# Performance work log

Hardware: AMD Instinct MI355X
Metric: run time of the kernel (lower is better)

## Reference

```python
import jax, jax.numpy as jnp
import numpy as np

VOCAB, HIDDEN, BATCH, TLEN = 32000, 512, 32, 64


def _lstm_cell(x, h, c, Wih, Whh, bih, bhh):
    # PyTorch LSTMCell gate order: i, f, g, o
    g = x @ Wih.T + bih + h @ Whh.T + bhh  # [B, 4H]
    i, f, gg, o = jnp.split(g, 4, axis=-1)
    i = jax.nn.sigmoid(i)
    f = jax.nn.sigmoid(f)
    gg = jnp.tanh(gg)
    o = jax.nn.sigmoid(o)
    c2 = f * c + i * gg
    h2 = o * jnp.tanh(c2)
    return h2, c2


def setup_inputs() -> dict:
    key = jax.random.key(0)
    ks = jax.random.split(key, 16)
    s = 0.02
    inp = {
        "inputs": jax.random.randint(ks[0], (1, BATCH), 0, VOCAB),
        "hiddens": jax.random.normal(ks[1], (BATCH, HIDDEN), jnp.float32),
        "target_sequences": jax.random.randint(ks[2], (BATCH, TLEN), 0, VOCAB),
        "use_tf": 1,
        "emb": jax.random.normal(ks[3], (VOCAB, HIDDEN), jnp.float32) * s,
        "W_ih1": jax.random.normal(ks[4], (4 * HIDDEN, HIDDEN), jnp.float32) * s,
        "W_hh1": jax.random.normal(ks[5], (4 * HIDDEN, HIDDEN), jnp.float32) * s,
        "b_ih1": jax.random.normal(ks[6], (4 * HIDDEN,), jnp.float32) * s,
        "b_hh1": jax.random.normal(ks[7], (4 * HIDDEN,), jnp.float32) * s,
        "W_ih2": jax.random.normal(ks[8], (4 * HIDDEN, HIDDEN), jnp.float32) * s,
        "W_hh2": jax.random.normal(ks[9], (4 * HIDDEN, HIDDEN), jnp.float32) * s,
        "b_ih2": jax.random.normal(ks[10], (4 * HIDDEN,), jnp.float32) * s,
        "b_hh2": jax.random.normal(ks[11], (4 * HIDDEN,), jnp.float32) * s,
        "W_out": jax.random.normal(ks[12], (VOCAB, HIDDEN), jnp.float32) * s,
        "b_out": jax.random.normal(ks[13], (VOCAB,), jnp.float32) * s,
    }
    return inp


def reference(inputs, hiddens, target_sequences, use_tf, emb, W_ih1, W_hh1,
              b_ih1, b_hh1, W_ih2, W_hh2, b_ih2, b_hh2, W_out, b_out):
    # Teacher-forcing path (use_tf is a static Python int; dropout p=0 -> identity).
    B = inputs.shape[1]
    H = hiddens.shape[1]
    # step i consumes: emb(inputs) for i=0, emb(target[:, i-1]) for i>0
    e0 = emb[inputs[0]]                              # [B, H]
    et = emb[target_sequences.T[:-1]]                # [T-1, B, H]
    x_seq = jnp.concatenate([e0[None], et], axis=0)  # [T, B, H]

    c1 = jnp.zeros((B, H), hiddens.dtype)
    h2 = jnp.zeros((B, H), hiddens.dtype)
    c2 = jnp.zeros((B, H), hiddens.dtype)

    def step(carry, x):
        h1, c1, h2, c2 = carry
        h1, c1 = _lstm_cell(x, h1, c1, W_ih1, W_hh1, b_ih1, b_hh1)
        h2, c2 = _lstm_cell(h1, h2, c2, W_ih2, W_hh2, b_ih2, b_hh2)
        probs = jax.nn.softmax(h2 @ W_out.T + b_out, axis=-1)  # [B, V]
        return (h1, c1, h2, c2), probs

    (h1, c1, h2, c2), output = jax.lax.scan(step, (hiddens, c1, h2, c2), x_seq)
    return output, h1  # output: [T, B, V]
```

## Files before the change

kernel.cpp:

```cpp
#include <hip/hip_runtime.h>
#include <stdint.h>


constexpr int kH = 512;
constexpr int kB = 32;
constexpr int kT = 64;
constexpr int kV = 32000;
constexpr int kG = 2048;
constexpr int kNWG = 256;
constexpr int kWS = 129;

typedef __attribute__((ext_vector_type(4))) float f4;
typedef __attribute__((ext_vector_type(8))) short short8;
typedef unsigned long long u64;

struct us4 { unsigned short x, y, z, w; };

__device__ inline unsigned short f2bf(float x) {
  union { float f; unsigned u; } c; c.f = x;
  unsigned r = c.u + 0x7fffu + ((c.u >> 16) & 1u);
  return (unsigned short)(r >> 16);
}
__device__ inline float sigm(float x) { return 1.0f / (1.0f + expf(-x)); }

__global__ void k_init(float* __restrict__ buf2, float* __restrict__ rowsum,
                       int* __restrict__ flags ) {
  int id = blockIdx.x * 256 + threadIdx.x;
  f4 z = {0.f, 0.f, 0.f, 0.f};
  if (id < 8192) ((f4*)buf2)[id] = z;
  if (id < 2048) rowsum[id] = 0.f;
  if (id < 512)  flags[id] = 0;
}

__global__ void k_wcvt(const float* __restrict__ W, unsigned short* __restrict__ Wu) {
  const int total = kV * kH / 4;
  for (int i = blockIdx.x * blockDim.x + threadIdx.x; i < total;
       i += gridDim.x * blockDim.x) {
    f4 v = ((const f4*)W)[i];
    us4 o = {f2bf(v.x), f2bf(v.y), f2bf(v.z), f2bf(v.w)};
    ((us4*)Wu)[i] = o;
  }
}

__global__ __launch_bounds__(256) void k_xg1(
    const int* __restrict__ inputs, const int* __restrict__ tseq,
    const float* __restrict__ emb, const float* __restrict__ Wih1,
    const float* __restrict__ bih1, const float* __restrict__ bhh1,
    float* __restrict__ Xg1T) {
  __shared__ float Xs[kB * kH];
  int tid = threadIdx.x;
  int t = blockIdx.x, jb = blockIdx.y;
  for (int i = tid; i < kB * kH / 4; i += 256) {
    int b = i >> 7;
    int tok = (t == 0) ? inputs[b] : tseq[b * kT + (t - 1)];
    ((f4*)Xs)[i] = ((const f4*)(emb + (size_t)tok * kH))[i & 127];
  }
  __syncthreads();
  int j2 = tid & 31, bq = tid >> 5;
  int j0 = jb * 64 + j2 * 2;
  int b0 = bq * 4;
  const f4* w0 = (const f4*)(Wih1 + (size_t)j0 * kH);
  const f4* w1 = (const f4*)(Wih1 + (size_t)(j0 + 1) * kH);
  float acc0[4] = {0.f, 0.f, 0.f, 0.f};
  float acc1[4] = {0.f, 0.f, 0.f, 0.f};
  #pragma unroll 2
  for (int k4 = 0; k4 < 128; ++k4) {
    f4 a0 = w0[k4], a1 = w1[k4];
    #pragma unroll
    for (int bb = 0; bb < 4; ++bb) {
      f4 x = ((const f4*)Xs)[(b0 + bb) * 128 + k4];
      acc0[bb] += a0.x * x.x + a0.y * x.y + a0.z * x.z + a0.w * x.w;
      acc1[bb] += a1.x * x.x + a1.y * x.y + a1.z * x.z + a1.w * x.w;
    }
  }
  float bj0 = bih1[j0] + bhh1[j0];
  float bj1 = bih1[j0 + 1] + bhh1[j0 + 1];
  f4 s0 = {acc0[0] + bj0, acc0[1] + bj0, acc0[2] + bj0, acc0[3] + bj0};
  f4 s1 = {acc1[0] + bj1, acc1[1] + bj1, acc1[2] + bj1, acc1[3] + bj1};
  float* o = Xg1T + ((size_t)t * kG + j0) * kB + b0;
  *(f4*)o = s0;
  *(f4*)(o + kB) = s1;
}

__device__ inline void postc(int* cnt) {
  __syncthreads();
  if (threadIdx.x == 0)
    __hip_atomic_fetch_add(cnt, 1, __ATOMIC_RELAXED, __HIP_MEMORY_SCOPE_AGENT);
}
__device__ inline void waitc(int* cnt, int target) {
  if (threadIdx.x == 0) {
    while (__hip_atomic_load(cnt, __ATOMIC_RELAXED,
                             __HIP_MEMORY_SCOPE_AGENT) < target)
      __builtin_amdgcn_s_sleep(2);
  }
  __syncthreads();
}

__device__ inline void stage_coh(float* __restrict__ smem, const float* src) {
  const u64* s8 = (const u64*)src;
  #pragma unroll
  for (int i = 0; i < 16; ++i) {
    int idx = threadIdx.x + (i << 8);
    u64 lo = __hip_atomic_load((u64*)&s8[idx * 2], __ATOMIC_RELAXED,
                               __HIP_MEMORY_SCOPE_AGENT);
    u64 hi = __hip_atomic_load((u64*)&s8[idx * 2 + 1], __ATOMIC_RELAXED,
                               __HIP_MEMORY_SCOPE_AGENT);
    int b_ = idx >> 7, k4 = idx & 127;
    union { u64 u[2]; f4 v; } cv; cv.u[0] = lo; cv.u[1] = hi;
    ((f4*)smem)[(b_ << 7) + (k4 ^ (b_ & 7))] = cv.v;
  }
}
__device__ inline void stage_plain(float* __restrict__ smem,
                                   const float* __restrict__ src) {
  const f4* s4 = (const f4*)src;
  #pragma unroll
  for (int i = 0; i < 16; ++i) {
    int idx = threadIdx.x + (i << 8);
    int b_ = idx >> 7, k4 = idx & 127;
    ((f4*)smem)[(b_ << 7) + (k4 ^ (b_ & 7))] = s4[idx];
  }
}

__global__ __launch_bounds__(256) void k_serial(
    const float* __restrict__ hiddens, const float* __restrict__ Xg1T,
    const float* __restrict__ Whh1, const float* __restrict__ Wih2,
    const float* __restrict__ Whh2, const float* __restrict__ bih2,
    const float* __restrict__ bhh2,
    float* __restrict__ buf1, float* __restrict__ buf2,
    unsigned short* __restrict__ H2u, float* __restrict__ outTail,
    int* __restrict__ cntA, int* __restrict__ cntB) {
  __shared__ float smemh[kB * kH];
  __shared__ float wlds[24 * 4 * kWS];
  const int tid = threadIdx.x, w = blockIdx.x;
  const int lane = tid & 63;
  const int b = tid >> 3, jj = tid & 7, gg = jj >> 1, nl = jj & 1;
  const int n = (w << 1) + nl;
  const int j = (gg << 9) + n;
  const float bias2 = bih2[j] + bhh2[j];
  const bool holder = (jj < 2);
  const int srcbase = (lane & 56) | (lane & 1);
  float c1 = 0.f, c2 = 0.f;
  const int boff = b << 7, bsw = b & 7;

  {
    f4* wl = (f4*)wlds;
    #pragma unroll
    for (int i = 0; i < 12; ++i) {
      int idx = tid + (i << 8);
      int row = idx >> 7, k4 = idx & 127;
      int m = row >> 3, jjr = row & 7;
      int jr = ((jjr >> 1) << 9) + (w << 1) + (jjr & 1);
      const float* src = (m == 0) ? Whh1 : (m == 1) ? Whh2 : Wih2;
      wl[row * kWS + k4] = ((const f4*)(src + (size_t)jr * kH))[k4];
    }
  }
  const f4* wl1  = (const f4*)wlds + (0 * 8 + jj) * kWS;
  const f4* wl2b = (const f4*)wlds + (1 * 8 + jj) * kWS;
  const f4* wl2a = (const f4*)wlds + (2 * 8 + jj) * kWS;
  const f4* hsm  = (const f4*)smemh;

  stage_plain(smemh, hiddens);
  __syncthreads();
  for (int t = 0; t < kT; ++t) {
    float* h1w = buf1 + (t & 1) * 16384;
    float* h2w = buf2 + (t & 1) * 16384;
    const float* h2r = buf2 + ((t + 1) & 1) * 16384;

    float xg = Xg1T[((size_t)t * kG + j) * kB + b];
    f4 acc = {0.f, 0.f, 0.f, 0.f};
    #pragma unroll 8
    for (int k4 = 0; k4 < 128; ++k4)
      acc += wl1[k4] * hsm[boff + (k4 ^ bsw)];
    float g1v = acc.x + acc.y + acc.z + acc.w + xg;
    float gi = __shfl(g1v, srcbase);
    float gf = __shfl(g1v, srcbase + 2);
    float gG = __shfl(g1v, srcbase + 4);
    float go = __shfl(g1v, srcbase + 6);
    float hnew = 0.f;
    if (holder) {
      float i_ = sigm(gi), f_ = sigm(gf), G_ = tanhf(gG), o_ = sigm(go);
      c1 = f_ * c1 + i_ * G_;
      hnew = o_ * tanhf(c1);
    }
    float hp = __shfl(hnew, lane + 1);
    if (jj == 0) {
      union { float f[2]; u64 u; } pk; pk.f[0] = hnew; pk.f[1] = hp;
      __hip_atomic_store((u64*)(h1w + b * kH + 2 * w), pk.u, __ATOMIC_RELAXED,
                         __HIP_MEMORY_SCOPE_AGENT);
      if (t == kT - 1) *(u64*)(outTail + b * kH + 2 * w) = pk.u;
    }
    postc(cntA);
    waitc(cntB, 256 * t);

    stage_coh(smemh, h2r);
    __syncthreads();
    f4 a2 = {0.f, 0.f, 0.f, 0.f};
    #pragma unroll 8
    for (int k4 = 0; k4 < 128; ++k4)
      a2 += wl2b[k4] * hsm[boff + (k4 ^ bsw)];
    waitc(cntA, 256 * (t + 1));

    stage_coh(smemh, h1w);
    __syncthreads();
    #pragma unroll 8
    for (int k4 = 0; k4 < 128; ++k4)
      a2 += wl2a[k4] * hsm[boff + (k4 ^ bsw)];
    float g2v = a2.x + a2.y + a2.z + a2.w + bias2;
    float g2i = __shfl(g2v, srcbase);
    float g2f = __shfl(g2v, srcbase + 2);
    float g2G = __shfl(g2v, srcbase + 4);
    float g2o = __shfl(g2v, srcbase + 6);
    float h2new = 0.f;
    if (holder) {
      float i_ = sigm(g2i), f_ = sigm(g2f), G_ = tanhf(g2G), o_ = sigm(g2o);
      c2 = f_ * c2 + i_ * G_;
      h2new = o_ * tanhf(c2);
    }
    float h2p = __shfl(h2new, lane + 1);
    if (jj == 0) {
      union { float f[2]; u64 u; } pk; pk.f[0] = h2new; pk.f[1] = h2p;
      __hip_atomic_store((u64*)(h2w + b * kH + 2 * w), pk.u, __ATOMIC_RELAXED,
                         __HIP_MEMORY_SCOPE_AGENT);
      unsigned bf2 = ((unsigned)f2bf(h2p) << 16) | f2bf(h2new);
      *(unsigned*)(H2u + ((size_t)t * kB + b) * kH + 2 * w) = bf2;
    }
    postc(cntB);
  }
}

__global__ __launch_bounds__(256) void k_vocab(
    const unsigned short* __restrict__ H2u, const unsigned short* __restrict__ Wu,
    const float* __restrict__ bout, float* __restrict__ out,
    float* __restrict__ rowsum) {
  const int lane = threadIdx.x & 63, wv = threadIdx.x >> 6;
  const int wm = wv >> 1, wn = wv & 1;
  const int r16 = lane & 15, quad = lane >> 4;
  const int mBase = blockIdx.y * 128 + wm * 64;
  const int nBase = blockIdx.x * 128 + wn * 64;
  f4 acc[4][4];
  #pragma unroll
  for (int a = 0; a < 4; ++a)
    #pragma unroll
    for (int c = 0; c < 4; ++c) acc[a][c] = (f4){0.f, 0.f, 0.f, 0.f};
  for (int kb = 0; kb < 16; ++kb) {
    int k0 = kb * 32 + quad * 8;
    short8 af[4], bf[4];
    #pragma unroll
    for (int mt = 0; mt < 4; ++mt)
      af[mt] = *(const short8*)(H2u + (size_t)(mBase + mt * 16 + r16) * kH + k0);
    #pragma unroll
    for (int nt = 0; nt < 4; ++nt)
      bf[nt] = *(const short8*)(Wu + (size_t)(nBase + nt * 16 + r16) * kH + k0);
    #pragma unroll
    for (int mt = 0; mt < 4; ++mt)
      #pragma unroll
      for (int nt = 0; nt < 4; ++nt)
        acc[mt][nt] = __builtin_amdgcn_mfma_f32_16x16x32_bf16(
            af[mt], bf[nt], acc[mt][nt], 0, 0, 0);
  }
  float bo[4];
  #pragma unroll
  for (int nt = 0; nt < 4; ++nt) bo[nt] = bout[nBase + nt * 16 + r16];
  #pragma unroll
  for (int mt = 0; mt < 4; ++mt) {
    #pragma unroll
    for (int r = 0; r < 4; ++r) {
      int row = mBase + mt * 16 + quad * 4 + r;
      float s = 0.f;
      #pragma unroll
      for (int nt = 0; nt < 4; ++nt) {
        float p = __expf(acc[mt][nt][r] + bo[nt]);
        out[(size_t)row * kV + nBase + nt * 16 + r16] = p;
        s += p;
      }
      s += __shfl_xor(s, 1);
      s += __shfl_xor(s, 2);
      s += __shfl_xor(s, 4);
      s += __shfl_xor(s, 8);
      if (r16 == 0) atomicAdd(&rowsum[row], s);
    }
  }
}

__global__ void k_scale(float* __restrict__ out, const float* __restrict__ rowsum) {
  const unsigned total4 = (unsigned)(kT * kB) * (kV / 4);
  unsigned stride = gridDim.x * blockDim.x;
  for (unsigned i = blockIdx.x * blockDim.x + threadIdx.x; i < total4; i += stride) {
    unsigned row = i / (kV / 4);
    float inv = 1.0f / rowsum[row];
    f4 v = ((const f4*)out)[i];
    ((f4*)out)[i] = v * inv;
  }
}

extern "C" void kernel_launch(void* const* d_in, const int* in_sizes, int n_in,
                              void* d_out, int out_size, void* d_ws, size_t ws_size,
                              hipStream_t stream) {
  (void)in_sizes; (void)n_in; (void)out_size; (void)ws_size;
  const int*   inputs  = (const int*)d_in[0];
  const float* hiddens = (const float*)d_in[1];
  const int*   tseq    = (const int*)d_in[2];
  const float* emb  = (const float*)d_in[4];
  const float* Wih1 = (const float*)d_in[5];
  const float* Whh1 = (const float*)d_in[6];
  const float* bih1 = (const float*)d_in[7];
  const float* bhh1 = (const float*)d_in[8];
  const float* Wih2 = (const float*)d_in[9];
  const float* Whh2 = (const float*)d_in[10];
  const float* bih2 = (const float*)d_in[11];
  const float* bhh2 = (const float*)d_in[12];
  const float* Wout = (const float*)d_in[13];
  const float* bout = (const float*)d_in[14];

  float* ws = (float*)d_ws;
  float* Xg1T = ws;
  float* buf1 = ws + 4194304;
  float* buf2 = ws + 4227072;
  unsigned short* H2u = (unsigned short*)(ws + 4259840);
  unsigned short* Wu  = (unsigned short*)(ws + 4784128);
  float* rowsum = ws + 12976128;
  int* flags = (int*)(ws + 12978176);
  int* cntA = flags;
  int* cntB = flags + 16;

  float* out = (float*)d_out;
  float* outTail = out + (size_t)kT * kB * kV;

  hipLaunchKernelGGL(k_init, dim3(32), dim3(256), 0, stream, buf2, rowsum, flags);
  hipLaunchKernelGGL(k_wcvt, dim3(1024), dim3(256), 0, stream, Wout, Wu);
  hipLaunchKernelGGL(k_xg1, dim3(64, 32), dim3(256), 0, stream,
                     inputs, tseq, emb, Wih1, bih1, bhh1, Xg1T);
  hipLaunchKernelGGL(k_serial, dim3(kNWG), dim3(256), 0, stream,
                     hiddens, Xg1T, Whh1, Wih2, Whh2, bih2, bhh2,
                     buf1, buf2, H2u, outTail, cntA, cntB);
  hipLaunchKernelGGL(k_vocab, dim3(kV / 128, 16), dim3(256), 0, stream,
                     H2u, Wu, bout, out, rowsum);
  hipLaunchKernelGGL(k_scale, dim3(2048), dim3(256), 0, stream, out, rowsum);
}
```

Measured before the change: 2.280 ms.

## Shard grid-barrier counters and re-map serial LSTM threads to k-split register tiles

The grid barrier counters are split into 8 padded slots, one per block group, so fewer blocks contend on each atomic. Waiters sum the slots with a wave-level reduction. The serial LSTM kernel's thread mapping is also restructured: each thread now covers all four gates for two batch rows over a 1/8 slice of K, and partial sums are combined with xor-shuffles. The remapping removes the shuffles that gathered gates from other lanes and the idle non-holder lanes, and it reuses each hidden-state load across four weight rows, at the cost of more registers and a change to the cntB offset.

```diff
diff --git a/kernel.cpp b/kernel.cpp
--- a/kernel.cpp
+++ b/kernel.cpp
@@ -85,13 +85,23 @@
 __device__ inline void postc(int* cnt) {
   __syncthreads();
   if (threadIdx.x == 0)
-    __hip_atomic_fetch_add(cnt, 1, __ATOMIC_RELAXED, __HIP_MEMORY_SCOPE_AGENT);
+    __hip_atomic_fetch_add(&cnt[(blockIdx.x & 7) << 5], 1, __ATOMIC_RELAXED,
+                           __HIP_MEMORY_SCOPE_AGENT);
 }
 __device__ inline void waitc(int* cnt, int target) {
-  if (threadIdx.x == 0) {
-    while (__hip_atomic_load(cnt, __ATOMIC_RELAXED,
-                             __HIP_MEMORY_SCOPE_AGENT) < target)
+  if (threadIdx.x < 64) {
+    int lane = threadIdx.x;
+    for (;;) {
+      int v = (lane < 8)
+                  ? __hip_atomic_load(&cnt[lane << 5], __ATOMIC_RELAXED,
+                                      __HIP_MEMORY_SCOPE_AGENT)
+                  : 0;
+      v += __shfl_xor(v, 1);
+      v += __shfl_xor(v, 2);
+      v += __shfl_xor(v, 4);
+      if (__shfl(v, 0) >= target) break;
       __builtin_amdgcn_s_sleep(2);
+    }
   }
   __syncthreads();
 }
@@ -121,7 +131,14 @@
   }
 }
 
-__global__ __launch_bounds__(256) void k_serial(
+__device__ inline float redk(float s) {
+  s += __shfl_xor(s, 1);
+  s += __shfl_xor(s, 2);
+  s += __shfl_xor(s, 4);
+  return s;
+}
+
+__global__ __launch_bounds__(256, 1) void k_serial(
     const float* __restrict__ hiddens, const float* __restrict__ Xg1T,
     const float* __restrict__ Whh1, const float* __restrict__ Wih2,
     const float* __restrict__ Whh2, const float* __restrict__ bih2,
@@ -132,15 +149,16 @@
   __shared__ float smemh[kB * kH];
   __shared__ float wlds[24 * 4 * kWS];
   const int tid = threadIdx.x, w = blockIdx.x;
-  const int lane = tid & 63;
-  const int b = tid >> 3, jj = tid & 7, gg = jj >> 1, nl = jj & 1;
+  const int lane = tid & 63, wv = tid >> 6;
+  const int ks = lane & 7;
+  const int nl = (lane >> 3) & 1;
+  const int bq = lane >> 4;
+  const int bp = (wv << 2) | bq;
+  const int b0 = bp << 1, b1 = b0 + 1;
+  const int b0off = b0 << 7, b1off = b1 << 7;
+  const int b0sw = b0 & 7, b1sw = b1 & 7;
+  const int kbase = ks << 4;
   const int n = (w << 1) + nl;
-  const int j = (gg << 9) + n;
-  const float bias2 = bih2[j] + bhh2[j];
-  const bool holder = (jj < 2);
-  const int srcbase = (lane & 56) | (lane & 1);
-  float c1 = 0.f, c2 = 0.f;
-  const int boff = b << 7, bsw = b & 7;
 
   {
     f4* wl = (f4*)wlds;
@@ -154,10 +172,24 @@
       wl[row * kWS + k4] = ((const f4*)(src + (size_t)jr * kH))[k4];
     }
   }
-  const f4* wl1  = (const f4*)wlds + (0 * 8 + jj) * kWS;
-  const f4* wl2b = (const f4*)wlds + (1 * 8 + jj) * kWS;
-  const f4* wl2a = (const f4*)wlds + (2 * 8 + jj) * kWS;
-  const f4* hsm  = (const f4*)smemh;
+  const f4* wr_hh1[4];
+  const f4* wr_hh2[4];
+  const f4* wr_ih2[4];
+  #pragma unroll
+  for (int gg = 0; gg < 4; ++gg) {
+    int row = 2 * gg + nl;
+    wr_hh1[gg] = (const f4*)wlds + (0 * 8 + row) * kWS;
+    wr_hh2[gg] = (const f4*)wlds + (1 * 8 + row) * kWS;
+    wr_ih2[gg] = (const f4*)wlds + (2 * 8 + row) * kWS;
+  }
+  float bj[4];
+  #pragma unroll
+  for (int gg = 0; gg < 4; ++gg)
+    bj[gg] = bih2[(gg << 9) + n] + bhh2[(gg << 9) + n];
+
+  const f4* hsm = (const f4*)smemh;
+  float c1a = 0.f, c1b = 0.f, c2a = 0.f, c2b = 0.f;
+  const f4 z4 = {0.f, 0.f, 0.f, 0.f};
 
   stage_plain(smemh, hiddens);
   __syncthreads();
@@ -166,63 +198,114 @@
     float* h2w = buf2 + (t & 1) * 16384;
     const float* h2r = buf2 + ((t + 1) & 1) * 16384;
 
-    float xg = Xg1T[((size_t)t * kG + j) * kB + b];
-    f4 acc = {0.f, 0.f, 0.f, 0.f};
-    #pragma unroll 8
-    for (int k4 = 0; k4 < 128; ++k4)
-      acc += wl1[k4] * hsm[boff + (k4 ^ bsw)];
-    float g1v = acc.x + acc.y + acc.z + acc.w + xg;
-    float gi = __shfl(g1v, srcbase);
-    float gf = __shfl(g1v, srcbase + 2);
-    float gG = __shfl(g1v, srcbase + 4);
-    float go = __shfl(g1v, srcbase + 6);
-    float hnew = 0.f;
-    if (holder) {
-      float i_ = sigm(gi), f_ = sigm(gf), G_ = tanhf(gG), o_ = sigm(go);
-      c1 = f_ * c1 + i_ * G_;
-      hnew = o_ * tanhf(c1);
-    }
-    float hp = __shfl(hnew, lane + 1);
-    if (jj == 0) {
-      union { float f[2]; u64 u; } pk; pk.f[0] = hnew; pk.f[1] = hp;
-      __hip_atomic_store((u64*)(h1w + b * kH + 2 * w), pk.u, __ATOMIC_RELAXED,
+    union { u64 u; float f[2]; } xv[4];
+    const float* xbase = Xg1T + ((size_t)t * kG + n) * kB + b0;
+    #pragma unroll
+    for (int gg = 0; gg < 4; ++gg)
+      xv[gg].u = *(const u64*)(xbase + (size_t)(gg << 9) * kB);
+
+    f4 a00 = z4, a01 = z4, a10 = z4, a11 = z4, a20 = z4, a21 = z4,
+       a30 = z4, a31 = z4;
+    #pragma unroll 4
+    for (int kk = 0; kk < 16; ++kk) {
+      int k4 = kbase + kk;
+      f4 h0v = hsm[b0off + (k4 ^ b0sw)];
+      f4 h1v = hsm[b1off + (k4 ^ b1sw)];
+      f4 w0 = wr_hh1[0][k4], w1 = wr_hh1[1][k4];
+      f4 w2 = wr_hh1[2][k4], w3 = wr_hh1[3][k4];
+      a00 += w0 * h0v; a01 += w0 * h1v;
+      a10 += w1 * h0v; a11 += w1 * h1v;
+      a20 += w2 * h0v; a21 += w2 * h1v;
+      a30 += w3 * h0v; a31 += w3 * h1v;
+    }
+    float G00 = redk(a00.x + a00.y + a00.z + a00.w) + xv[0].f[0];
+    float G01 = redk(a01.x + a01.y + a01.z + a01.w) + xv[0].f[1];
+    float G10 = redk(a10.x + a10.y + a10.z + a10.w) + xv[1].f[0];
+    float G11 = redk(a11.x + a11.y + a11.z + a11.w) + xv[1].f[1];
+    float G20 = redk(a20.x + a20.y + a20.z + a20.w) + xv[2].f[0];
+    float G21 = redk(a21.x + a21.y + a21.z + a21.w) + xv[2].f[1];
+    float G30 = redk(a30.x + a30.y + a30.z + a30.w) + xv[3].f[0];
+    float G31 = redk(a31.x + a31.y + a31.z + a31.w) + xv[3].f[1];
+    c1a = sigm(G10) * c1a + sigm(G00) * tanhf(G20);
+    float hn0 = sigm(G30) * tanhf(c1a);
+    c1b = sigm(G11) * c1b + sigm(G01) * tanhf(G21);
+    float hn1 = sigm(G31) * tanhf(c1b);
+    float hp0 = __shfl(hn0, lane ^ 8);
+    float hp1 = __shfl(hn1, lane ^ 8);
+    if ((lane & 15) == 0) {
+      union { float f[2]; u64 u; } p0, p1;
+      p0.f[0] = hn0; p0.f[1] = hp0;
+      p1.f[0] = hn1; p1.f[1] = hp1;
+      __hip_atomic_store((u64*)(h1w + b0 * kH + 2 * w), p0.u, __ATOMIC_RELAXED,
                          __HIP_MEMORY_SCOPE_AGENT);
-      if (t == kT - 1) *(u64*)(outTail + b * kH + 2 * w) = pk.u;
+      __hip_atomic_store((u64*)(h1w + b1 * kH + 2 * w), p1.u, __ATOMIC_RELAXED,
+                         __HIP_MEMORY_SCOPE_AGENT);
+      if (t == kT - 1) {
+        *(u64*)(outTail + b0 * kH + 2 * w) = p0.u;
+        *(u64*)(outTail + b1 * kH + 2 * w) = p1.u;
+      }
     }
     postc(cntA);
     waitc(cntB, 256 * t);
 
     stage_coh(smemh, h2r);
     __syncthreads();
-    f4 a2 = {0.f, 0.f, 0.f, 0.f};
-    #pragma unroll 8
-    for (int k4 = 0; k4 < 128; ++k4)
-      a2 += wl2b[k4] * hsm[boff + (k4 ^ bsw)];
+    a00 = z4; a01 = z4; a10 = z4; a11 = z4;
+    a20 = z4; a21 = z4; a30 = z4; a31 = z4;
+    #pragma unroll 4
+    for (int kk = 0; kk < 16; ++kk) {
+      int k4 = kbase + kk;
+      f4 h0v = hsm[b0off + (k4 ^ b0sw)];
+      f4 h1v = hsm[b1off + (k4 ^ b1sw)];
+      f4 w0 = wr_hh2[0][k4], w1 = wr_hh2[1][k4];
+      f4 w2 = wr_hh2[2][k4], w3 = wr_hh2[3][k4];
+      a00 += w0 * h0v; a01 += w0 * h1v;
+      a10 += w1 * h0v; a11 += w1 * h1v;
+      a20 += w2 * h0v; a21 += w2 * h1v;
+      a30 += w3 * h0v; a31 += w3 * h1v;
+    }
     waitc(cntA, 256 * (t + 1));
 
     stage_coh(smemh, h1w);
     __syncthreads();
-    #pragma unroll 8
-    for (int k4 = 0; k4 < 128; ++k4)
-      a2 += wl2a[k4] * hsm[boff + (k4 ^ bsw)];
-    float g2v = a2.x + a2.y + a2.z + a2.w + bias2;
-    float g2i = __shfl(g2v, srcbase);
-    float g2f = __shfl(g2v, srcbase + 2);
-    float g2G = __shfl(g2v, srcbase + 4);
-    float g2o = __shfl(g2v, srcbase + 6);
-    float h2new = 0.f;
-    if (holder) {
-      float i_ = sigm(g2i), f_ = sigm(g2f), G_ = tanhf(g2G), o_ = sigm(g2o);
-      c2 = f_ * c2 + i_ * G_;
-      h2new = o_ * tanhf(c2);
-    }
-    float h2p = __shfl(h2new, lane + 1);
-    if (jj == 0) {
-      union { float f[2]; u64 u; } pk; pk.f[0] = h2new; pk.f[1] = h2p;
-      __hip_atomic_store((u64*)(h2w + b * kH + 2 * w), pk.u, __ATOMIC_RELAXED,
+    #pragma unroll 4
+    for (int kk = 0; kk < 16; ++kk) {
+      int k4 = kbase + kk;
+      f4 h0v = hsm[b0off + (k4 ^ b0sw)];
+      f4 h1v = hsm[b1off + (k4 ^ b1sw)];
+      f4 w0 = wr_ih2[0][k4], w1 = wr_ih2[1][k4];
+      f4 w2 = wr_ih2[2][k4], w3 = wr_ih2[3][k4];
+      a00 += w0 * h0v; a01 += w0 * h1v;
+      a10 += w1 * h0v; a11 += w1 * h1v;
+      a20 += w2 * h0v; a21 += w2 * h1v;
+      a30 += w3 * h0v; a31 += w3 * h1v;
+    }
+    G00 = redk(a00.x + a00.y + a00.z + a00.w) + bj[0];
+    G01 = redk(a01.x + a01.y + a01.z + a01.w) + bj[0];
+    G10 = redk(a10.x + a10.y + a10.z + a10.w) + bj[1];
+    G11 = redk(a11.x + a11.y + a11.z + a11.w) + bj[1];
+    G20 = redk(a20.x + a20.y + a20.z + a20.w) + bj[2];
+    G21 = redk(a21.x + a21.y + a21.z + a21.w) + bj[2];
+    G30 = redk(a30.x + a30.y + a30.z + a30.w) + bj[3];
+    G31 = redk(a31.x + a31.y + a31.z + a31.w) + bj[3];
+    c2a = sigm(G10) * c2a + sigm(G00) * tanhf(G20);
+    float h2n0 = sigm(G30) * tanhf(c2a);
+    c2b = sigm(G11) * c2b + sigm(G01) * tanhf(G21);
+    float h2n1 = sigm(G31) * tanhf(c2b);
+    float h2p0 = __shfl(h2n0, lane ^ 8);
+    float h2p1 = __shfl(h2n1, lane ^ 8);
+    if ((lane & 15) == 0) {
+      union { float f[2]; u64 u; } p0, p1;
+      p0.f[0] = h2n0; p0.f[1] = h2p0;
+      p1.f[0] = h2n1; p1.f[1] = h2p1;
+      __hip_atomic_store((u64*)(h2w + b0 * kH + 2 * w), p0.u, __ATOMIC_RELAXED,
                          __HIP_MEMORY_SCOPE_AGENT);
-      unsigned bf2 = ((unsigned)f2bf(h2p) << 16) | f2bf(h2new);
-      *(unsigned*)(H2u + ((size_t)t * kB + b) * kH + 2 * w) = bf2;
+      __hip_atomic_store((u64*)(h2w + b1 * kH + 2 * w), p1.u, __ATOMIC_RELAXED,
+                         __HIP_MEMORY_SCOPE_AGENT);
+      unsigned bf0 = ((unsigned)f2bf(h2p0) << 16) | f2bf(h2n0);
+      unsigned bf1 = ((unsigned)f2bf(h2p1) << 16) | f2bf(h2n1);
+      *(unsigned*)(H2u + ((size_t)t * kB + b0) * kH + 2 * w) = bf0;
+      *(unsigned*)(H2u + ((size_t)t * kB + b1) * kH + 2 * w) = bf1;
     }
     postc(cntB);
   }
@@ -321,7 +404,7 @@
   float* rowsum = ws + 12976128;
   int* flags = (int*)(ws + 12978176);
   int* cntA = flags;
-  int* cntB = flags + 16;
+  int* cntB = flags + 256;
 
   float* out = (float*)d_out;
   float* outTail = out + (size_t)kT * kB * kV;
```

New measurement: 2.773 ms. 1.22x slower.
